# Optimization experiments

Hardware: AMD Instinct MI355X
Metric: run time of the kernel (lower is better)

The kernel has to match this reference:

```python
import jax, jax.numpy as jnp
import numpy as np

EPS = 1e-8
NUM_HEADS = 8
SCALE = 25.0
SIM_THRESH = 0.75
BLOCK = 10  # per-frame proposal group size used by the zeroing mask


def _l2norm(x):
    return x / (jnp.linalg.norm(x, axis=-1, keepdims=True) + EPS)


def setup_inputs() -> dict:
    key = jax.random.key(0)
    ks = jax.random.split(key, 7)
    B, N, C = 1, 2000, 256
    H = NUM_HEADS
    x_cls = jax.random.normal(ks[0], (B, N, C), dtype=jnp.float32)
    x_reg = jax.random.normal(ks[1], (B, N, C), dtype=jnp.float32)
    cls_score = jax.random.uniform(ks[2], (N,), dtype=jnp.float32)
    fg_score = jax.random.uniform(ks[3], (N,), dtype=jnp.float32)
    coord_attn = jax.random.uniform(ks[4], (B, H, N, N), dtype=jnp.float32)
    W_qkv_cls = jax.random.normal(ks[5], (3 * C, C), dtype=jnp.float32) * 0.02
    W_qkv_reg = jax.random.normal(ks[6], (3 * C, C), dtype=jnp.float32) * 0.02
    return {"x_cls": x_cls, "x_reg": x_reg, "cls_score": cls_score,
            "fg_score": fg_score, "coord_attn": coord_attn,
            "W_qkv_cls": W_qkv_cls, "W_qkv_reg": W_qkv_reg}


def reference(x_cls, x_reg, cls_score, fg_score, coord_attn, W_qkv_cls, W_qkv_reg):
    B, N, C = x_cls.shape
    H = NUM_HEADS
    D = C // H

    def qkv(x, W):
        t = (x @ W.T).reshape(B, N, 3, H, D).transpose(2, 0, 3, 1, 4)  # [3,B,H,N,D]
        return t[0], t[1], t[2]

    q_cls, k_cls, v_cls = qkv(x_cls, W_qkv_cls)
    q_reg, k_reg, v_reg = qkv(x_reg, W_qkv_reg)

    q_cls, k_cls = _l2norm(q_cls), _l2norm(k_cls)
    q_reg, k_reg = _l2norm(q_reg), _l2norm(k_reg)
    v_cls_normed = _l2norm(v_cls)

    cs = cls_score.reshape(1, 1, 1, N)  # broadcast over [B,H,N,N]
    fs = fg_score.reshape(1, 1, 1, N)

    attn_cls_raw = jnp.einsum('bhnd,bhmd->bhnm', v_cls_normed, v_cls_normed)

    attn_cls = jax.nn.softmax(jnp.einsum('bhnd,bhmd->bhnm', q_cls, k_cls) * SCALE * cs, axis=-1)
    attn_reg = jax.nn.softmax(jnp.einsum('bhnd,bhmd->bhnm', q_reg, k_reg) * SCALE * fs, axis=-1)

    attn = (attn_reg + attn_cls) * 0.5 * coord_attn
    attn = jax.lax.stop_gradient(attn)  # original detaches before masking

    # block-diagonal zeroing: row j zeros cols [j//10*10, j//10*10+9), keep diagonal
    rows = jnp.arange(N)[:, None]
    cols = jnp.arange(N)[None, :]
    block_start = (rows // BLOCK) * BLOCK
    zero_mask = (cols >= block_start) & (cols < block_start + (BLOCK - 1)) & (cols != rows)
    attn = jnp.where(zero_mask, 0.0, attn)

    x = jnp.einsum('bhnm,bhmd->bhnd', attn, v_cls).transpose(0, 2, 1, 3).reshape(B, N, C)
    x_ori = v_cls.transpose(0, 2, 1, 3).reshape(B, N, C)
    x_cat = jnp.concatenate([x, x_ori], axis=-1)  # [B,N,2C]

    # ave=True branch
    sim_raw = jnp.sum(attn_cls_raw, axis=1)[0] / H          # [N,N]
    sim_mask = (sim_raw > SIM_THRESH).astype(x_cls.dtype)
    sim_attn = jnp.sum(attn, axis=1)[0] / H                 # [N,N]
    sim_round2 = jax.nn.softmax(sim_attn, axis=-1)
    sim_round2 = sim_mask * sim_round2 / (jnp.sum(sim_mask * sim_round2, axis=-1, keepdims=True) + EPS)
    return x_cat, sim_round2
```

## Files before the change

### kernel.cpp

```cpp
#include <hip/hip_runtime.h>
#include <math.h>

typedef _Float16 half8 __attribute__((ext_vector_type(8)));
typedef _Float16 half4 __attribute__((ext_vector_type(4)));
typedef float f32x4 __attribute__((ext_vector_type(4)));

constexpr int N = 2000;
constexpr int NP = 2048;
constexpr int H = 8;
constexpr int D = 32;
constexpr float SCL = 25.0f;
constexpr float FM = 25.0f;

#define MFMA16(a,b,c)  __builtin_amdgcn_mfma_f32_16x16x32_f16((a),(b),(c),0,0,0)
#define MFMA16K(a,b,c) __builtin_amdgcn_mfma_f32_16x16x16f16((a),(b),(c),0,0,0)


__global__ __launch_bounds__(256) void wconv_kernel(
    const float* __restrict__ Wc, const float* __restrict__ Wr,
    _Float16* __restrict__ Wch, _Float16* __restrict__ Wrh)
{
    const int i = blockIdx.x * 256 + threadIdx.x;
    Wch[i] = (_Float16)Wc[i];
    Wrh[i] = (_Float16)Wr[i];
}

__global__ __launch_bounds__(256) void qkv_kernel(
    const float* __restrict__ xc, const float* __restrict__ xr,
    const _Float16* __restrict__ Wch, const _Float16* __restrict__ Wrh,
    _Float16* __restrict__ Qch, _Float16* __restrict__ Kch,
    _Float16* __restrict__ Qrh, _Float16* __restrict__ Krh,
    _Float16* __restrict__ Vnh, _Float16* __restrict__ Vth,
    float* __restrict__ out)
{
    constexpr int XS = 264;
    __shared__ _Float16 xs[16 * XS];
    const int t = threadIdx.x;
    const int n0 = blockIdx.x * 16;
    const int by = blockIdx.y;
    const int which = (by < 3) ? by : (by - 3);
    const bool isCls = by < 3;
    const float* x = isCls ? xc : xr;
    const _Float16* Wh = isCls ? Wch : Wrh;

    #pragma unroll
    for (int it = 0; it < 4; ++it) {
        const int f = t + it * 256;
        const int row = f >> 6, c4 = f & 63;
        const float4 v = *(const float4*)(x + (size_t)(n0 + row) * 256 + c4 * 4);
        half4 hv; hv[0]=(_Float16)v.x; hv[1]=(_Float16)v.y; hv[2]=(_Float16)v.z; hv[3]=(_Float16)v.w;
        *(half4*)&xs[row * XS + c4 * 4] = hv;
    }
    __syncthreads();

    const int w = t >> 6, l = t & 63;
    const int lr = l & 15, lg = l >> 4;
    const int obase = which * 256 + w * 64;
    f32x4 acc[4] = {{0,0,0,0},{0,0,0,0},{0,0,0,0},{0,0,0,0}};
    for (int k0 = 0; k0 < 256; k0 += 32) {
        const half8 aX = *(const half8*)&xs[lr * XS + k0 + lg * 8];
        #pragma unroll
        for (int s = 0; s < 4; ++s) {
            const half8 bW = *(const half8*)(Wh + (size_t)(obase + s * 16 + lr) * 256 + k0 + lg * 8);
            acc[s] = MFMA16(aX, bW, acc[s]);
        }
    }
    #pragma unroll
    for (int p = 0; p < 2; ++p) {
        const int h = 2 * w + p;
        float ss[4];
        #pragma unroll
        for (int j = 0; j < 4; ++j) {
            float v = acc[2*p][j]*acc[2*p][j] + acc[2*p+1][j]*acc[2*p+1][j];
            #pragma unroll
            for (int off = 1; off < 16; off <<= 1) v += __shfl_xor(v, off);
            ss[j] = sqrtf(v) + 1e-8f;
        }
        if (which < 2) {
            _Float16* Qd = isCls ? (which == 0 ? Qch : Kch) : (which == 0 ? Qrh : Krh);
            #pragma unroll
            for (int sh = 0; sh < 2; ++sh)
                #pragma unroll
                for (int j = 0; j < 4; ++j)
                    Qd[((size_t)h*NP + n0 + lg*4 + j)*D + sh*16 + lr] = (_Float16)(acc[2*p+sh][j] / ss[j]);
        } else {
            #pragma unroll
            for (int sh = 0; sh < 2; ++sh) {
                const int d = sh * 16 + lr;
                half4 tv;
                #pragma unroll
                for (int j = 0; j < 4; ++j) {
                    const float raw = acc[2*p+sh][j];
                    Vnh[((size_t)h*NP + n0 + lg*4 + j)*D + d] = (_Float16)(raw / ss[j]);
                    out[(size_t)(n0 + lg*4 + j)*512 + 256 + h*D + d] = raw;
                    tv[j] = (_Float16)raw;
                }
                *(half4*)(Vth + ((size_t)h*D + d)*NP + n0 + lg*4) = tv;
            }
        }
    }
}

__global__ __launch_bounds__(512) void stats_kernel(
    const _Float16* __restrict__ Qch, const _Float16* __restrict__ Kch,
    const _Float16* __restrict__ Qrh, const _Float16* __restrict__ Krh,
    const float* __restrict__ clsScore, const float* __restrict__ fgScore,
    float* __restrict__ STi)
{
    __shared__ float Ssh[4][2][16];
    const int t = threadIdx.x;
    const int w = t >> 6, l = t & 63;
    const int nsub = w >> 1, mhalf = w & 1;
    const int n0 = blockIdx.x * 64 + nsub * 16;
    const int h = blockIdx.y, z = blockIdx.z;
    const _Float16* Q = z ? Qrh : Qch;
    const _Float16* K = z ? Krh : Kch;
    const float* score = z ? fgScore : clsScore;
    const int lr = l & 15, lg = l >> 4;
    const half8 aQ = *(const half8*)(Q + ((size_t)h*NP + n0 + lr)*D + lg*8);
    float S[4] = {0.f, 0.f, 0.f, 0.f};
    const int msBeg = mhalf ? 63 : 0;
    const int msEnd = mhalf ? 125 : 63;
    for (int ms = msBeg; ms < msEnd; ++ms) {
        const int m = ms * 16 + lr;
        const half8 bK = *(const half8*)(K + ((size_t)h*NP + m)*D + lg*8);
        f32x4 z4 = {0.f, 0.f, 0.f, 0.f};
        const f32x4 c = MFMA16(aQ, bK, z4);
        const float sm = SCL * score[m];
        #pragma unroll
        for (int j = 0; j < 4; ++j) S[j] += __expf(fmaf(c[j], sm, -FM));
    }
    #pragma unroll
    for (int j = 0; j < 4; ++j) {
        #pragma unroll
        for (int off = 1; off < 16; off <<= 1) S[j] += __shfl_xor(S[j], off);
    }
    if (lr == 0) {
        #pragma unroll
        for (int j = 0; j < 4; ++j) Ssh[nsub][mhalf][lg*4 + j] = S[j];
    }
    __syncthreads();
    if (t < 64) {
        const int ns = t >> 4, rl = t & 15;
        STi[((size_t)z*H + h)*NP + blockIdx.x*64 + ns*16 + rl]
            = 1.f / (Ssh[ns][0][rl] + Ssh[ns][1][rl]);
    }
}

__global__ __launch_bounds__(256) void vvmask_kernel(
    const _Float16* __restrict__ Vnh, unsigned char* __restrict__ Mask)
{
    const int t = threadIdx.x;
    const int w = t >> 6, l = t & 63;
    const int n0 = blockIdx.y * 16;
    const int m00 = blockIdx.x * 256 + w * 64;
    const int lr = l & 15, lg = l >> 4;
    half8 aV[8];
    #pragma unroll
    for (int h = 0; h < 8; ++h)
        aV[h] = *(const half8*)(Vnh + ((size_t)(h*NP + n0 + lr))*D + lg*8);
    for (int s = 0; s < 4; ++s) {
        const int mb = m00 + s*16;
        f32x4 acc = {0.f, 0.f, 0.f, 0.f};
        #pragma unroll
        for (int h = 0; h < 8; ++h) {
            const half8 bV = *(const half8*)(Vnh + ((size_t)(h*NP + mb + lr))*D + lg*8);
            acc = MFMA16(aV[h], bV, acc);
        }
        const int m = mb + lr;
        if (m < N) {
            #pragma unroll
            for (int j = 0; j < 4; ++j) {
                const int n = n0 + lg*4 + j;
                Mask[(size_t)n*N + m] = (acc[j]*0.125f > 0.75f) ? (unsigned char)1 : (unsigned char)0;
            }
        }
    }
}

__global__ __launch_bounds__(256) void attn_kernel(
    const _Float16* __restrict__ Qch, const _Float16* __restrict__ Kch,
    const _Float16* __restrict__ Qrh, const _Float16* __restrict__ Krh,
    const _Float16* __restrict__ Vth, const float* __restrict__ coord,
    const float* __restrict__ clsScore, const float* __restrict__ fgScore,
    const float* __restrict__ STi,
    float* __restrict__ SIM, _Float16* __restrict__ XPH)
{
    __shared__ _Float16 pvred[2][4][2][16][18];

    const int t = threadIdx.x;
    const int w = t >> 6, l = t & 63;
    const int lr = l & 15, lg = l >> 4;
    const int mc = blockIdx.x;
    const int m0 = mc * 128;
    const int n0 = blockIdx.y * 16;
    const int n  = n0 + lr;
    const int bs = (n / 10) * 10;
    const int cb = w * 32;

    int mb[2]; bool ok[2];
    #pragma unroll
    for (int s = 0; s < 2; ++s) { mb[s] = m0 + cb + s*16; ok[s] = mb[s] < N; }

    f32x4 sc4[2], sf4[2];
    #pragma unroll
    for (int s = 0; s < 2; ++s) {
        sc4[s] = ok[s] ? SCL * *(const f32x4*)(clsScore + mb[s] + lg*4) : (f32x4){0,0,0,0};
        sf4[s] = ok[s] ? SCL * *(const f32x4*)(fgScore  + mb[s] + lg*4) : (f32x4){0,0,0,0};
    }
    float simacc[2][4] = {{0,0,0,0},{0,0,0,0}};

    for (int h = 0; h < H; ++h) {
        const float iC = STi[((size_t)0*H + h)*NP + n];
        const float iR = STi[((size_t)1*H + h)*NP + n];
        const half8 aQc = *(const half8*)(Qch + ((size_t)h*NP + n)*D + lg*8);
        const half8 aQr = *(const half8*)(Qrh + ((size_t)h*NP + n)*D + lg*8);

        f32x4 pvA[2][2] = {{{0,0,0,0},{0,0,0,0}},{{0,0,0,0},{0,0,0,0}}};
        #pragma unroll
        for (int s = 0; s < 2; ++s) {
            if (!ok[s]) continue;
            const half8 bKc = *(const half8*)(Kch + ((size_t)h*NP + mb[s] + lr)*D + lg*8);
            const half8 bKr = *(const half8*)(Krh + ((size_t)h*NP + mb[s] + lr)*D + lg*8);
            const f32x4 co = *(const f32x4*)(coord + ((size_t)h*N + n)*N + mb[s] + lg*4);
            f32x4 z4 = {0.f,0.f,0.f,0.f};
            const f32x4 cc = MFMA16(bKc, aQc, z4);
            const f32x4 cr = MFMA16(bKr, aQr, z4);
            half4 af;
            #pragma unroll
            for (int j = 0; j < 4; ++j) {
                const int m = mb[s] + lg*4 + j;
                float a = (__expf(fmaf(cc[j], sc4[s][j], -FM)) * iC
                         + __expf(fmaf(cr[j], sf4[s][j], -FM)) * iR) * 0.5f * co[j];
                if (m >= bs && m < bs+9 && m != n) a = 0.f;
                simacc[s][j] += a;
                af[j] = (_Float16)a;
            }
            const half4 bV0 = *(const half4*)(Vth + ((size_t)h*D + lr)*NP + mb[s] + lg*4);
            const half4 bV1 = *(const half4*)(Vth + ((size_t)h*D + 16 + lr)*NP + mb[s] + lg*4);
            pvA[s][0] = MFMA16K(af, bV0, pvA[s][0]);
            pvA[s][1] = MFMA16K(af, bV1, pvA[s][1]);
        }
        const f32x4 pv0 = pvA[0][0] + pvA[1][0];
        const f32x4 pv1 = pvA[0][1] + pvA[1][1];

        const int buf = h & 1;
        half4 h0, h1;
        #pragma unroll
        for (int j = 0; j < 4; ++j) { h0[j] = (_Float16)pv0[j]; h1[j] = (_Float16)pv1[j]; }
        *(half4*)&pvred[buf][w][0][lr][lg*4] = h0;
        *(half4*)&pvred[buf][w][1][lr][lg*4] = h1;
        __syncthreads();
        const size_t xbase = ((size_t)(mc*H + h)*N + n0)*D;
        #pragma unroll
        for (int e = t; e < 512; e += 256) {
            const int d = e & 15, db = (e >> 4) & 1, q = e >> 5;
            const float sum = (float)pvred[buf][0][db][d][q] + (float)pvred[buf][1][db][d][q]
                            + (float)pvred[buf][2][db][d][q] + (float)pvred[buf][3][db][d][q];
            XPH[xbase + e] = (_Float16)sum;
        }
    }

    #pragma unroll
    for (int s = 0; s < 2; ++s) {
        if (!ok[s]) continue;
        f32x4 v;
        #pragma unroll
        for (int j = 0; j < 4; ++j) v[j] = simacc[s][j] * 0.125f;
        *(f32x4*)(SIM + (size_t)n*N + mb[s] + lg*4) = v;
    }
}

__global__ __launch_bounds__(256) void reduce_kernel(
    const _Float16* __restrict__ XPH, float* __restrict__ out)
{
    const int n = blockIdx.x, t = threadIdx.x;
    const int h = t >> 5, d = t & 31;
    float acc = 0.f;
    #pragma unroll
    for (int mcI = 0; mcI < 16; ++mcI)
        acc += (float)XPH[(((size_t)mcI*H + h)*N + n)*D + d];
    out[(size_t)n*512 + t] = acc;
}

__global__ __launch_bounds__(256) void simfinal_kernel(
    const float* __restrict__ SIM, const unsigned char* __restrict__ Mask,
    float* __restrict__ out)
{
    __shared__ float4 buf[500];
    __shared__ float redA[4], redB[4];
    const int n = blockIdx.x, t = threadIdx.x;
    const float4* row4 = (const float4*)(SIM + (size_t)n*N);
    const uchar4* mrow4 = (const uchar4*)(Mask + (size_t)n*N);
    float mx = -1e30f;
    for (int i = t; i < 500; i += 256) {
        const float4 v = row4[i];
        buf[i] = v;
        mx = fmaxf(mx, fmaxf(fmaxf(v.x, v.y), fmaxf(v.z, v.w)));
    }
    #pragma unroll
    for (int off = 1; off < 64; off <<= 1) mx = fmaxf(mx, __shfl_xor(mx, off));
    const int wv = t >> 6;
    if ((t & 63) == 0) redA[wv] = mx;
    __syncthreads();
    const float M = fmaxf(fmaxf(redA[0], redA[1]), fmaxf(redA[2], redA[3]));
    float sA = 0.f, sM = 0.f;
    for (int i = t; i < 500; i += 256) {
        float4 v = buf[i];
        const uchar4 mk = mrow4[i];
        v.x = __expf(v.x - M); v.y = __expf(v.y - M);
        v.z = __expf(v.z - M); v.w = __expf(v.w - M);
        buf[i] = v;
        sA += v.x + v.y + v.z + v.w;
        sM += (mk.x ? v.x : 0.f) + (mk.y ? v.y : 0.f) + (mk.z ? v.z : 0.f) + (mk.w ? v.w : 0.f);
    }
    #pragma unroll
    for (int off = 1; off < 64; off <<= 1) { sA += __shfl_xor(sA, off); sM += __shfl_xor(sM, off); }
    __syncthreads();
    if ((t & 63) == 0) { redA[wv] = sA; redB[wv] = sM; }
    __syncthreads();
    const float SA = redA[0] + redA[1] + redA[2] + redA[3];
    const float SMK = redB[0] + redB[1] + redB[2] + redB[3];
    const float inv = 1.f / (SMK + 1e-8f * SA);
    float4* orow = (float4*)(out + 1024000 + (size_t)n*N);
    for (int i = t; i < 500; i += 256) {
        const float4 v = buf[i];
        const uchar4 mk = mrow4[i];
        orow[i] = make_float4(mk.x ? v.x * inv : 0.f, mk.y ? v.y * inv : 0.f,
                              mk.z ? v.z * inv : 0.f, mk.w ? v.w * inv : 0.f);
    }
}

extern "C" void kernel_launch(void* const* d_in, const int* in_sizes, int n_in,
                              void* d_out, int out_size, void* d_ws, size_t ws_size,
                              hipStream_t stream) {
    const float* x_cls     = (const float*)d_in[0];
    const float* x_reg     = (const float*)d_in[1];
    const float* cls_score = (const float*)d_in[2];
    const float* fg_score  = (const float*)d_in[3];
    const float* coord     = (const float*)d_in[4];
    const float* Wc        = (const float*)d_in[5];
    const float* Wr        = (const float*)d_in[6];

    char* base = (char*)d_ws;
    float* STi      = (float*)base;
    float* SIM      = (float*)(base + 131072);
    _Float16* XPH   = (_Float16*)(base + 16131072);
    _Float16* Qch   = (_Float16*)(base + 32515072);
    _Float16* Kch   = Qch + 524288;
    _Float16* Qrh   = Qch + 2*524288;
    _Float16* Krh   = Qch + 3*524288;
    _Float16* Vnh   = Qch + 4*524288;
    _Float16* Vth   = Qch + 5*524288;
    _Float16* Wch   = (_Float16*)(base + 38806528);
    _Float16* Wrh   = (_Float16*)(base + 39199744);
    unsigned char* Mask = (unsigned char*)(base + 39592960);
    float* out = (float*)d_out;

    wconv_kernel<<<768, 256, 0, stream>>>(Wc, Wr, Wch, Wrh);
    qkv_kernel<<<dim3(125, 5), 256, 0, stream>>>(x_cls, x_reg, Wch, Wrh,
                                                 Qch, Kch, Qrh, Krh, Vnh, Vth, out);
    stats_kernel<<<dim3(32, 8, 2), 512, 0, stream>>>(Qch, Kch, Qrh, Krh, cls_score, fg_score, STi);
    vvmask_kernel<<<dim3(8, 125), 256, 0, stream>>>(Vnh, Mask);
    attn_kernel<<<dim3(16, 125), 256, 0, stream>>>(Qch, Kch, Qrh, Krh, Vth, coord,
                                                   cls_score, fg_score, STi, SIM, XPH);
    reduce_kernel<<<2000, 256, 0, stream>>>(XPH, out);
    simfinal_kernel<<<2000, 256, 0, stream>>>(SIM, Mask, out);
}
```

Measured before the change: 142.4 us.

## Prefetch heads in attention, store sim matrix as fp16, use exp2

```diff
diff --git a/kernel.cpp b/kernel.cpp
--- a/kernel.cpp
+++ b/kernel.cpp
@@ -3,6 +3,7 @@
 
 typedef _Float16 half8 __attribute__((ext_vector_type(8)));
 typedef _Float16 half4 __attribute__((ext_vector_type(4)));
+typedef _Float16 half2v __attribute__((ext_vector_type(2)));
 typedef float f32x4 __attribute__((ext_vector_type(4)));
 
 constexpr int N = 2000;
@@ -10,10 +11,13 @@
 constexpr int H = 8;
 constexpr int D = 32;
 constexpr float SCL = 25.0f;
-constexpr float FM = 25.0f;
+constexpr float L2E = 1.4426950408889634f;
+constexpr float FM2 = 25.0f * L2E;
 
 #define MFMA16(a,b,c)  __builtin_amdgcn_mfma_f32_16x16x32_f16((a),(b),(c),0,0,0)
 #define MFMA16K(a,b,c) __builtin_amdgcn_mfma_f32_16x16x16f16((a),(b),(c),0,0,0)
+
+__device__ __forceinline__ float fexp2(float x) { return __builtin_amdgcn_exp2f(x); }
 
 
 __global__ __launch_bounds__(256) void wconv_kernel(
@@ -121,14 +125,20 @@
     float S[4] = {0.f, 0.f, 0.f, 0.f};
     const int msBeg = mhalf ? 63 : 0;
     const int msEnd = mhalf ? 125 : 63;
+    half8 bK = *(const half8*)(K + ((size_t)h*NP + msBeg*16 + lr)*D + lg*8);
+    float sc = score[msBeg*16 + lr];
     for (int ms = msBeg; ms < msEnd; ++ms) {
-        const int m = ms * 16 + lr;
-        const half8 bK = *(const half8*)(K + ((size_t)h*NP + m)*D + lg*8);
+        const half8 cur = bK;
+        const float scc = sc;
+        if (ms + 1 < msEnd) {
+            bK = *(const half8*)(K + ((size_t)h*NP + (ms+1)*16 + lr)*D + lg*8);
+            sc = score[(ms+1)*16 + lr];
+        }
         f32x4 z4 = {0.f, 0.f, 0.f, 0.f};
-        const f32x4 c = MFMA16(aQ, bK, z4);
-        const float sm = SCL * score[m];
-        #pragma unroll
-        for (int j = 0; j < 4; ++j) S[j] += __expf(fmaf(c[j], sm, -FM));
+        const f32x4 c = MFMA16(aQ, cur, z4);
+        const float sm2 = scc * (SCL * L2E);
+        #pragma unroll
+        for (int j = 0; j < 4; ++j) S[j] += fexp2(fmaf(c[j], sm2, -FM2));
     }
     #pragma unroll
     for (int j = 0; j < 4; ++j) {
@@ -178,13 +188,20 @@
     }
 }
 
+struct Stage {
+    half8 aQc, aQr;
+    half8 bKc[2], bKr[2];
+    f32x4 co[2];
+    float iC, iR;
+};
+
 __global__ __launch_bounds__(256) void attn_kernel(
     const _Float16* __restrict__ Qch, const _Float16* __restrict__ Kch,
     const _Float16* __restrict__ Qrh, const _Float16* __restrict__ Krh,
     const _Float16* __restrict__ Vth, const float* __restrict__ coord,
     const float* __restrict__ clsScore, const float* __restrict__ fgScore,
     const float* __restrict__ STi,
-    float* __restrict__ SIM, _Float16* __restrict__ XPH)
+    _Float16* __restrict__ SIMH, _Float16* __restrict__ XPH)
 {
     __shared__ _Float16 pvred[2][4][2][16][18];
 
@@ -205,69 +222,93 @@
     f32x4 sc4[2], sf4[2];
     #pragma unroll
     for (int s = 0; s < 2; ++s) {
-        sc4[s] = ok[s] ? SCL * *(const f32x4*)(clsScore + mb[s] + lg*4) : (f32x4){0,0,0,0};
-        sf4[s] = ok[s] ? SCL * *(const f32x4*)(fgScore  + mb[s] + lg*4) : (f32x4){0,0,0,0};
+        sc4[s] = ok[s] ? (SCL*L2E) * *(const f32x4*)(clsScore + mb[s] + lg*4) : (f32x4){0,0,0,0};
+        sf4[s] = ok[s] ? (SCL*L2E) * *(const f32x4*)(fgScore  + mb[s] + lg*4) : (f32x4){0,0,0,0};
     }
     float simacc[2][4] = {{0,0,0,0},{0,0,0,0}};
 
-    for (int h = 0; h < H; ++h) {
-        const float iC = STi[((size_t)0*H + h)*NP + n];
-        const float iR = STi[((size_t)1*H + h)*NP + n];
-        const half8 aQc = *(const half8*)(Qch + ((size_t)h*NP + n)*D + lg*8);
-        const half8 aQr = *(const half8*)(Qrh + ((size_t)h*NP + n)*D + lg*8);
-
+    auto loadStage = [&](int h, Stage& st) {
+        st.iC = STi[(size_t)h*NP + n];
+        st.iR = STi[((size_t)(H + h))*NP + n];
+        st.aQc = *(const half8*)(Qch + ((size_t)h*NP + n)*D + lg*8);
+        st.aQr = *(const half8*)(Qrh + ((size_t)h*NP + n)*D + lg*8);
+        #pragma unroll
+        for (int s = 0; s < 2; ++s) {
+            if (ok[s]) {
+                st.bKc[s] = *(const half8*)(Kch + ((size_t)h*NP + mb[s] + lr)*D + lg*8);
+                st.bKr[s] = *(const half8*)(Krh + ((size_t)h*NP + mb[s] + lr)*D + lg*8);
+                st.co[s]  = *(const f32x4*)(coord + ((size_t)h*N + n)*N + mb[s] + lg*4);
+            }
+        }
+    };
+
+    auto computeHead = [&](int h, const Stage& st) {
+        half4 bV0[2], bV1[2];
+        #pragma unroll
+        for (int s = 0; s < 2; ++s) if (ok[s]) {
+            bV0[s] = *(const half4*)(Vth + ((size_t)(h*D + lr))*NP + mb[s] + lg*4);
+            bV1[s] = *(const half4*)(Vth + ((size_t)(h*D + 16 + lr))*NP + mb[s] + lg*4);
+        }
         f32x4 pvA[2][2] = {{{0,0,0,0},{0,0,0,0}},{{0,0,0,0},{0,0,0,0}}};
         #pragma unroll
         for (int s = 0; s < 2; ++s) {
             if (!ok[s]) continue;
-            const half8 bKc = *(const half8*)(Kch + ((size_t)h*NP + mb[s] + lr)*D + lg*8);
-            const half8 bKr = *(const half8*)(Krh + ((size_t)h*NP + mb[s] + lr)*D + lg*8);
-            const f32x4 co = *(const f32x4*)(coord + ((size_t)h*N + n)*N + mb[s] + lg*4);
             f32x4 z4 = {0.f,0.f,0.f,0.f};
-            const f32x4 cc = MFMA16(bKc, aQc, z4);
-            const f32x4 cr = MFMA16(bKr, aQr, z4);
+            const f32x4 cc = MFMA16(st.bKc[s], st.aQc, z4);
+            const f32x4 cr = MFMA16(st.bKr[s], st.aQr, z4);
             half4 af;
             #pragma unroll
             for (int j = 0; j < 4; ++j) {
                 const int m = mb[s] + lg*4 + j;
-                float a = (__expf(fmaf(cc[j], sc4[s][j], -FM)) * iC
-                         + __expf(fmaf(cr[j], sf4[s][j], -FM)) * iR) * 0.5f * co[j];
+                float a = (fexp2(fmaf(cc[j], sc4[s][j], -FM2)) * st.iC
+                         + fexp2(fmaf(cr[j], sf4[s][j], -FM2)) * st.iR) * 0.5f * st.co[s][j];
                 if (m >= bs && m < bs+9 && m != n) a = 0.f;
                 simacc[s][j] += a;
                 af[j] = (_Float16)a;
             }
-            const half4 bV0 = *(const half4*)(Vth + ((size_t)h*D + lr)*NP + mb[s] + lg*4);
-            const half4 bV1 = *(const half4*)(Vth + ((size_t)h*D + 16 + lr)*NP + mb[s] + lg*4);
-            pvA[s][0] = MFMA16K(af, bV0, pvA[s][0]);
-            pvA[s][1] = MFMA16K(af, bV1, pvA[s][1]);
+            pvA[s][0] = MFMA16K(af, bV0[s], pvA[s][0]);
+            pvA[s][1] = MFMA16K(af, bV1[s], pvA[s][1]);
         }
         const f32x4 pv0 = pvA[0][0] + pvA[1][0];
         const f32x4 pv1 = pvA[0][1] + pvA[1][1];
-
         const int buf = h & 1;
         half4 h0, h1;
         #pragma unroll
         for (int j = 0; j < 4; ++j) { h0[j] = (_Float16)pv0[j]; h1[j] = (_Float16)pv1[j]; }
         *(half4*)&pvred[buf][w][0][lr][lg*4] = h0;
         *(half4*)&pvred[buf][w][1][lr][lg*4] = h1;
-        __syncthreads();
+        asm volatile("s_waitcnt lgkmcnt(0)" ::: "memory");
+        __builtin_amdgcn_s_barrier();
         const size_t xbase = ((size_t)(mc*H + h)*N + n0)*D;
-        #pragma unroll
-        for (int e = t; e < 512; e += 256) {
-            const int d = e & 15, db = (e >> 4) & 1, q = e >> 5;
-            const float sum = (float)pvred[buf][0][db][d][q] + (float)pvred[buf][1][db][d][q]
-                            + (float)pvred[buf][2][db][d][q] + (float)pvred[buf][3][db][d][q];
-            XPH[xbase + e] = (_Float16)sum;
-        }
+        {
+            const int e0 = 2*t;
+            const int d = e0 & 15, db = (e0 >> 4) & 1, q = e0 >> 5;
+            const float s0 = (float)pvred[buf][0][db][d][q]   + (float)pvred[buf][1][db][d][q]
+                           + (float)pvred[buf][2][db][d][q]   + (float)pvred[buf][3][db][d][q];
+            const float s1 = (float)pvred[buf][0][db][d+1][q] + (float)pvred[buf][1][db][d+1][q]
+                           + (float)pvred[buf][2][db][d+1][q] + (float)pvred[buf][3][db][d+1][q];
+            half2v o; o[0] = (_Float16)s0; o[1] = (_Float16)s1;
+            *(half2v*)(XPH + xbase + e0) = o;
+        }
+    };
+
+    Stage A, B;
+    loadStage(0, A);
+    #pragma unroll
+    for (int hp = 0; hp < H; hp += 2) {
+        loadStage(hp + 1, B);
+        computeHead(hp, A);
+        if (hp + 2 < H) loadStage(hp + 2, A);
+        computeHead(hp + 1, B);
     }
 
     #pragma unroll
     for (int s = 0; s < 2; ++s) {
         if (!ok[s]) continue;
-        f32x4 v;
-        #pragma unroll
-        for (int j = 0; j < 4; ++j) v[j] = simacc[s][j] * 0.125f;
-        *(f32x4*)(SIM + (size_t)n*N + mb[s] + lg*4) = v;
+        half4 v;
+        #pragma unroll
+        for (int j = 0; j < 4; ++j) v[j] = (_Float16)(simacc[s][j] * 0.125f);
+        *(half4*)(SIMH + (size_t)n*N + mb[s] + lg*4) = v;
     }
 }
 
@@ -284,19 +325,23 @@
 }
 
 __global__ __launch_bounds__(256) void simfinal_kernel(
-    const float* __restrict__ SIM, const unsigned char* __restrict__ Mask,
+    const _Float16* __restrict__ SIMH, const unsigned char* __restrict__ Mask,
     float* __restrict__ out)
 {
-    __shared__ float4 buf[500];
     __shared__ float redA[4], redB[4];
     const int n = blockIdx.x, t = threadIdx.x;
-    const float4* row4 = (const float4*)(SIM + (size_t)n*N);
-    const uchar4* mrow4 = (const uchar4*)(Mask + (size_t)n*N);
+    const _Float16* row = SIMH + (size_t)n * N;
+    const unsigned char* mrow = Mask + (size_t)n * N;
+    const bool act = t < 250;
+    float f[8];
+    unsigned int mk0 = 0, mk1 = 0;
     float mx = -1e30f;
-    for (int i = t; i < 500; i += 256) {
-        const float4 v = row4[i];
-        buf[i] = v;
-        mx = fmaxf(mx, fmaxf(fmaxf(v.x, v.y), fmaxf(v.z, v.w)));
+    if (act) {
+        const half8 v8 = *(const half8*)(row + t*8);
+        const uint2 mm = *(const uint2*)(mrow + t*8);
+        mk0 = mm.x; mk1 = mm.y;
+        #pragma unroll
+        for (int k = 0; k < 8; ++k) { f[k] = (float)v8[k]; mx = fmaxf(mx, f[k]); }
     }
     #pragma unroll
     for (int off = 1; off < 64; off <<= 1) mx = fmaxf(mx, __shfl_xor(mx, off));
@@ -304,15 +349,16 @@
     if ((t & 63) == 0) redA[wv] = mx;
     __syncthreads();
     const float M = fmaxf(fmaxf(redA[0], redA[1]), fmaxf(redA[2], redA[3]));
+    float e[8];
     float sA = 0.f, sM = 0.f;
-    for (int i = t; i < 500; i += 256) {
-        float4 v = buf[i];
-        const uchar4 mk = mrow4[i];
-        v.x = __expf(v.x - M); v.y = __expf(v.y - M);
-        v.z = __expf(v.z - M); v.w = __expf(v.w - M);
-        buf[i] = v;
-        sA += v.x + v.y + v.z + v.w;
-        sM += (mk.x ? v.x : 0.f) + (mk.y ? v.y : 0.f) + (mk.z ? v.z : 0.f) + (mk.w ? v.w : 0.f);
+    if (act) {
+        #pragma unroll
+        for (int k = 0; k < 8; ++k) {
+            e[k] = fexp2((f[k] - M) * L2E);
+            sA += e[k];
+            const unsigned int mkb = ((k < 4 ? mk0 : mk1) >> (8*(k & 3))) & 0xffu;
+            if (mkb) sM += e[k]; else e[k] = 0.f;
+        }
     }
     #pragma unroll
     for (int off = 1; off < 64; off <<= 1) { sA += __shfl_xor(sA, off); sM += __shfl_xor(sM, off); }
@@ -322,12 +368,10 @@
     const float SA = redA[0] + redA[1] + redA[2] + redA[3];
     const float SMK = redB[0] + redB[1] + redB[2] + redB[3];
     const float inv = 1.f / (SMK + 1e-8f * SA);
-    float4* orow = (float4*)(out + 1024000 + (size_t)n*N);
-    for (int i = t; i < 500; i += 256) {
-        const float4 v = buf[i];
-        const uchar4 mk = mrow4[i];
-        orow[i] = make_float4(mk.x ? v.x * inv : 0.f, mk.y ? v.y * inv : 0.f,
-                              mk.z ? v.z * inv : 0.f, mk.w ? v.w * inv : 0.f);
+    if (act) {
+        float* orow = out + 1024000 + (size_t)n*N + t*8;
+        *(float4*)(orow)     = make_float4(e[0]*inv, e[1]*inv, e[2]*inv, e[3]*inv);
+        *(float4*)(orow + 4) = make_float4(e[4]*inv, e[5]*inv, e[6]*inv, e[7]*inv);
     }
 }
 
@@ -344,17 +388,17 @@
 
     char* base = (char*)d_ws;
     float* STi      = (float*)base;
-    float* SIM      = (float*)(base + 131072);
-    _Float16* XPH   = (_Float16*)(base + 16131072);
-    _Float16* Qch   = (_Float16*)(base + 32515072);
+    _Float16* SIMH  = (_Float16*)(base + 131072);
+    _Float16* XPH   = (_Float16*)(base + 8131072);
+    _Float16* Qch   = (_Float16*)(base + 24515072);
     _Float16* Kch   = Qch + 524288;
     _Float16* Qrh   = Qch + 2*524288;
     _Float16* Krh   = Qch + 3*524288;
     _Float16* Vnh   = Qch + 4*524288;
     _Float16* Vth   = Qch + 5*524288;
-    _Float16* Wch   = (_Float16*)(base + 38806528);
-    _Float16* Wrh   = (_Float16*)(base + 39199744);
-    unsigned char* Mask = (unsigned char*)(base + 39592960);
+    _Float16* Wch   = (_Float16*)(base + 30806528);
+    _Float16* Wrh   = (_Float16*)(base + 31199744);
+    unsigned char* Mask = (unsigned char*)(base + 31592960);
     float* out = (float*)d_out;
 
     wconv_kernel<<<768, 256, 0, stream>>>(Wc, Wr, Wch, Wrh);
@@ -363,7 +407,7 @@
     stats_kernel<<<dim3(32, 8, 2), 512, 0, stream>>>(Qch, Kch, Qrh, Krh, cls_score, fg_score, STi);
     vvmask_kernel<<<dim3(8, 125), 256, 0, stream>>>(Vnh, Mask);
     attn_kernel<<<dim3(16, 125), 256, 0, stream>>>(Qch, Kch, Qrh, Krh, Vth, coord,
-                                                   cls_score, fg_score, STi, SIM, XPH);
+                                                   cls_score, fg_score, STi, SIMH, XPH);
     reduce_kernel<<<2000, 256, 0, stream>>>(XPH, out);
-    simfinal_kernel<<<2000, 256, 0, stream>>>(SIM, Mask, out);
-}
+    simfinal_kernel<<<2000, 256, 0, stream>>>(SIMH, Mask, out);
+}
```

New measurement: 142.2 us. Within noise of the previous version (-0.2%).
